# Kernel tuning notes

Hardware: AMD Instinct MI355X
Metric: run time of the kernel (lower is better)

## Reference

```python
import jax, jax.numpy as jnp
import numpy as np

B, S, D, H = 2, 2048, 1024, 16
HD = D // H  # head_dim = 64


def setup_inputs() -> dict:
    key = jax.random.key(0)
    ks = jax.random.split(key, 6)
    scale = D ** -0.5
    x = jax.random.normal(ks[0], (B, S, D), dtype=jnp.float32)
    wq = jax.random.normal(ks[1], (D, D), dtype=jnp.float32) * scale
    wk = jax.random.normal(ks[2], (D, D), dtype=jnp.float32) * scale
    wv = jax.random.normal(ks[3], (D, D), dtype=jnp.float32) * scale
    wo = jax.random.normal(ks[4], (D, D), dtype=jnp.float32) * scale
    # RoPE frequencies: theta_i = 10000^(-2i/HD), angles[t, i] = t * theta_i
    inv_freq = 1.0 / (10000.0 ** (np.arange(0, HD, 2, dtype=np.float32) / HD))
    t = np.arange(S, dtype=np.float32)
    angles = np.outer(t, inv_freq)  # [S, HD//2]
    freqs_cos = jnp.asarray(np.cos(angles), dtype=jnp.float32)
    freqs_sin = jnp.asarray(np.sin(angles), dtype=jnp.float32)
    # additive causal mask [1,1,S,S]
    neg = jnp.float32(-1e9)
    mask = jnp.triu(jnp.full((S, S), neg, dtype=jnp.float32), k=1)[None, None]
    return {"x": x, "wq": wq, "wk": wk, "wv": wv, "wo": wo,
            "freqs_cos": freqs_cos, "freqs_sin": freqs_sin,
            "mask": mask, "start_pos": 0}


def _apply_rope(q, freqs_cos, freqs_sin):
    # q: [B, S, H, HD] -> pairs (even, odd) rotated by angle per position
    b, s, h, hd = q.shape
    q2 = q.reshape(b, s, h, hd // 2, 2)
    qr, qi = q2[..., 0], q2[..., 1]
    c = freqs_cos[None, :, None, :]  # [1, S, 1, HD//2]
    sn = freqs_sin[None, :, None, :]
    out_r = qr * c - qi * sn
    out_i = qr * sn + qi * c
    return jnp.stack([out_r, out_i], axis=-1).reshape(b, s, h, hd)


def reference(x, wq, wk, wv, wo, freqs_cos, freqs_sin, mask, start_pos):
    b, s, _ = x.shape
    xq = (x @ wq).reshape(b, s, H, HD)
    xk = (x @ wk).reshape(b, s, H, HD)
    xv = (x @ wv).reshape(b, s, H, HD)
    xq = _apply_rope(xq, freqs_cos, freqs_sin)
    xk = _apply_rope(xk, freqs_cos, freqs_sin)
    # [B, H, S, HD]
    q = xq.transpose(0, 2, 1, 3)
    k = xk.transpose(0, 2, 1, 3)
    v = xv.transpose(0, 2, 1, 3)
    scores = jnp.einsum('bhqd,bhkd->bhqk', q, k) / jnp.sqrt(jnp.float32(HD))
    scores = scores + mask
    probs = jax.nn.softmax(scores.astype(jnp.float32), axis=-1).astype(q.dtype)
    out = jnp.einsum('bhqk,bhkd->bhqd', probs, v)
    out = out.transpose(0, 2, 1, 3).reshape(b, s, H * HD)
    return out @ wo
```

## Files before the change

### kernel.cpp

```cpp
#include <hip/hip_runtime.h>

typedef unsigned short u16;
typedef __bf16 bf16x8 __attribute__((ext_vector_type(8)));
typedef float f32x4 __attribute__((ext_vector_type(4)));

#define DD 1024
#define SS 2048
#define HH 16
#define HDIM 64

__device__ __forceinline__ u16 f2bf(float f) {
  union { float f; unsigned u; } x; x.f = f;
  unsigned r = x.u + 0x7FFFu + ((x.u >> 16) & 1u);
  return (u16)(r >> 16);
}

__device__ __forceinline__ void gload_lds16(const u16* g, u16* l) {
  __builtin_amdgcn_global_load_lds((const __attribute__((address_space(1))) void*)g,
                                   (__attribute__((address_space(3))) void*)l, 16, 0, 0);
}

__global__ __launch_bounds__(256) void cvt_x(const float* __restrict__ in, u16* __restrict__ out, int n) {
  int i = (blockIdx.x * 256 + threadIdx.x) * 4;
  if (i + 3 < n) {
    float4 v = *(const float4*)(in + i);
    out[i + 0] = f2bf(v.x);
    out[i + 1] = f2bf(v.y);
    out[i + 2] = f2bf(v.z);
    out[i + 3] = f2bf(v.w);
  }
}

__global__ __launch_bounds__(256) void transpose_w(const float* __restrict__ w0, const float* __restrict__ w1,
                                                   const float* __restrict__ w2, const float* __restrict__ w3,
                                                   u16* __restrict__ out) {
  __shared__ float t[32][33];
  const float* w = (blockIdx.z == 0) ? w0 : (blockIdx.z == 1) ? w1 : (blockIdx.z == 2) ? w2 : w3;
  u16* o = out + (size_t)blockIdx.z * DD * DD;
  int j0 = blockIdx.x * 32;
  int i0 = blockIdx.y * 32;
  int tx = threadIdx.x, ty = threadIdx.y;
#pragma unroll
  for (int r = ty; r < 32; r += 8)
    t[r][tx] = w[(size_t)(i0 + r) * DD + j0 + tx];
  __syncthreads();
#pragma unroll
  for (int r = ty; r < 32; r += 8)
    o[(size_t)(j0 + r) * DD + i0 + tx] = f2bf(t[tx][r]);
}

__device__ __forceinline__ void gemm_128(const u16* __restrict__ A, const u16* __restrict__ BT,
                                         int m0, int n0, int K, u16* As, u16* Bs, f32x4 acc[4][4]) {
  const int tid = threadIdx.x;
  const int lane = tid & 63;
  const int wid = tid >> 6;
  const int wm = wid >> 1, wn = wid & 1;
  const int lr = lane & 15;
  const int lg = lane >> 4;
#pragma unroll
  for (int i = 0; i < 4; ++i)
#pragma unroll
    for (int j = 0; j < 4; ++j)
      acc[i][j] = (f32x4){0.f, 0.f, 0.f, 0.f};

  for (int kt = 0; kt < K / 64; ++kt) {
    int k0 = kt * 64;
    __syncthreads();
#pragma unroll
    for (int i = 0; i < 4; ++i) {
      int c = i * 256 + tid;
      int row = c >> 3;
      int j = (c & 7) ^ (row & 7);
      gload_lds16(A + (size_t)(m0 + row) * K + k0 + j * 8, As + c * 8);
      gload_lds16(BT + (size_t)(n0 + row) * K + k0 + j * 8, Bs + c * 8);
    }
    __syncthreads();
#pragma unroll
    for (int ks = 0; ks < 2; ++ks) {
      bf16x8 af[4], bfr[4];
#pragma unroll
      for (int mi = 0; mi < 4; ++mi) {
        int row = wm * 64 + mi * 16 + lr;
        int ch = (ks * 4 + lg) ^ (row & 7);
        af[mi] = *(const bf16x8*)(As + row * 64 + ch * 8);
      }
#pragma unroll
      for (int ni = 0; ni < 4; ++ni) {
        int row = wn * 64 + ni * 16 + lr;
        int ch = (ks * 4 + lg) ^ (row & 7);
        bfr[ni] = *(const bf16x8*)(Bs + row * 64 + ch * 8);
      }
      __builtin_amdgcn_s_setprio(1);
#pragma unroll
      for (int mi = 0; mi < 4; ++mi)
#pragma unroll
        for (int ni = 0; ni < 4; ++ni)
          acc[mi][ni] = __builtin_amdgcn_mfma_f32_16x16x32_bf16(af[mi], bfr[ni], acc[mi][ni], 0, 0, 0);
      __builtin_amdgcn_s_setprio(0);
    }
  }
}

__global__ __launch_bounds__(256, 2) void gemm_qkv(const u16* __restrict__ xb, const u16* __restrict__ wT,
                                                   const float* __restrict__ fc, const float* __restrict__ fs,
                                                   u16* __restrict__ Qr, u16* __restrict__ Kr, u16* __restrict__ Vt) {
  __shared__ u16 As[128 * 64], Bs[128 * 64];
  const int z = blockIdx.z;
  const u16* BT = wT + (size_t)z * DD * DD;
  f32x4 acc[4][4];
  int m0 = blockIdx.x * 128, n0 = blockIdx.y * 128;
  gemm_128(xb, BT, m0, n0, DD, As, Bs, acc);

  const int lane = threadIdx.x & 63, wid = threadIdx.x >> 6;
  const int wm = wid >> 1, wn = wid & 1, lr = lane & 15, lg = lane >> 4;
#pragma unroll
  for (int mi = 0; mi < 4; ++mi)
#pragma unroll
    for (int ni = 0; ni < 4; ++ni)
#pragma unroll
      for (int j = 0; j < 4; ++j) {
        int m = m0 + wm * 64 + mi * 16 + lg * 4 + j;
        int n = n0 + wn * 64 + ni * 16 + lr;
        float v = acc[mi][ni][j];
        int b = m >> 11, s = m & 2047;
        int h = n >> 6, hd = n & 63;
        if (z == 2) {
          Vt[((size_t)(b * HH + h) * HDIM + hd) * SS + s] = f2bf(v);
        } else {
          float pv = __shfl_xor(v, 1);
          int fi = s * 32 + (hd >> 1);
          float c = fc[fi], sn = fs[fi];
          float o = ((hd & 1) == 0) ? (v * c - pv * sn) : (pv * sn + v * c);
          u16* dst = (z == 0) ? Qr : Kr;
          dst[((size_t)(b * HH + h) * SS + s) * HDIM + hd] = f2bf(o);
        }
      }
}

__global__ __launch_bounds__(256, 4) void attn(const u16* __restrict__ Qr, const u16* __restrict__ Kr,
                                               const u16* __restrict__ Vt, u16* __restrict__ Ob) {
  __shared__ u16 Kb[2][64 * 64];
  __shared__ u16 Vb[2][64 * 64];
  __shared__ u16 Ps[4][16 * 64];
  const int id = blockIdx.x;
  const int xcd = id & 7;
  const int r = id >> 3;
  const int qt = 31 - (r >> 2);
  const int bh = xcd * 4 + (r & 3);

  const u16* Qh = Qr + (size_t)bh * SS * HDIM;
  const u16* Kh = Kr + (size_t)bh * SS * HDIM;
  const u16* Vh = Vt + (size_t)bh * HDIM * SS;

  const int tid = threadIdx.x;
  const int lane = tid & 63, wid = tid >> 6;
  const int lr = lane & 15, lg = lane >> 4;
  const int q0 = qt * 64 + wid * 16;
  u16* Pw = &Ps[wid][0];

  const int c0 = tid, c1 = 256 + tid;
  const int srow0 = c0 >> 3, sj0 = (c0 & 7) ^ (srow0 & 7);
  const int srow1 = c1 >> 3, sj1 = (c1 & 7) ^ (srow1 & 7);

  bf16x8 aq[2];
#pragma unroll
  for (int ks = 0; ks < 2; ++ks)
    aq[ks] = *(const bf16x8*)(Qh + (q0 + lr) * HDIM + ks * 32 + lg * 8);

  bf16x8 ones;
  {
    union { u16 u[8]; bf16x8 v; } ou;
#pragma unroll
    for (int i = 0; i < 8; ++i) ou.u[i] = 0x3F80;
    ones = ou.v;
  }

  f32x4 o[4];
#pragma unroll
  for (int d = 0; d < 4; ++d) o[d] = (f32x4){0.f, 0.f, 0.f, 0.f};
  f32x4 ls = (f32x4){0.f, 0.f, 0.f, 0.f};

  gload_lds16(Kh + (size_t)srow0 * HDIM + sj0 * 8, &Kb[0][c0 * 8]);
  gload_lds16(Kh + (size_t)srow1 * HDIM + sj1 * 8, &Kb[0][c1 * 8]);
  gload_lds16(Vh + (size_t)srow0 * SS + sj0 * 8, &Vb[0][c0 * 8]);
  gload_lds16(Vh + (size_t)srow1 * SS + sj1 * 8, &Vb[0][c1 * 8]);

  for (int t = 0; t <= qt; ++t) {
    const int cur = t & 1;
    __syncthreads();

    if (t < qt) {
      const int g0 = (t + 1) * 64;
      gload_lds16(Kh + (size_t)(g0 + srow0) * HDIM + sj0 * 8, &Kb[cur ^ 1][c0 * 8]);
      gload_lds16(Kh + (size_t)(g0 + srow1) * HDIM + sj1 * 8, &Kb[cur ^ 1][c1 * 8]);
      gload_lds16(Vh + (size_t)srow0 * SS + g0 + sj0 * 8, &Vb[cur ^ 1][c0 * 8]);
      gload_lds16(Vh + (size_t)srow1 * SS + g0 + sj1 * 8, &Vb[cur ^ 1][c1 * 8]);
    }

    f32x4 sc[4];
#pragma unroll
    for (int kb = 0; kb < 4; ++kb) sc[kb] = (f32x4){0.f, 0.f, 0.f, 0.f};
    __builtin_amdgcn_s_setprio(1);
#pragma unroll
    for (int ks = 0; ks < 2; ++ks)
#pragma unroll
      for (int kb = 0; kb < 4; ++kb) {
        int row = kb * 16 + lr;
        int ch = (ks * 4 + lg) ^ (row & 7);
        bf16x8 bk = *(const bf16x8*)(&Kb[cur][row * 64 + ch * 8]);
        sc[kb] = __builtin_amdgcn_mfma_f32_16x16x32_bf16(aq[ks], bk, sc[kb], 0, 0, 0);
      }
    __builtin_amdgcn_s_setprio(0);

    if (t == qt) {
#pragma unroll
      for (int kb = 0; kb < 4; ++kb)
#pragma unroll
        for (int j = 0; j < 4; ++j) {
          int q = q0 + lg * 4 + j;
          int kk = t * 64 + kb * 16 + lr;
          float e = __expf(sc[kb][j] * 0.125f);
          sc[kb][j] = (kk > q) ? 0.f : e;
        }
    } else {
#pragma unroll
      for (int kb = 0; kb < 4; ++kb)
#pragma unroll
        for (int j = 0; j < 4; ++j)
          sc[kb][j] = __expf(sc[kb][j] * 0.125f);
    }

#pragma unroll
    for (int kb = 0; kb < 4; ++kb)
#pragma unroll
      for (int j = 0; j < 4; ++j) {
        int rr = lg * 4 + j;
        int ccol = kb * 16 + lr;
        int ch = (ccol >> 3) ^ (rr & 7);
        Pw[rr * 64 + ch * 8 + (ccol & 7)] = f2bf(sc[kb][j]);
      }
#pragma unroll
    for (int ks = 0; ks < 2; ++ks) {
      int chp = (ks * 4 + lg) ^ (lr & 7);
      bf16x8 ap = *(const bf16x8*)(Pw + lr * 64 + chp * 8);
      __builtin_amdgcn_s_setprio(1);
      ls = __builtin_amdgcn_mfma_f32_16x16x32_bf16(ap, ones, ls, 0, 0, 0);
#pragma unroll
      for (int d = 0; d < 4; ++d) {
        int row = d * 16 + lr;
        int ch = (ks * 4 + lg) ^ (row & 7);
        bf16x8 bv = *(const bf16x8*)(&Vb[cur][row * 64 + ch * 8]);
        o[d] = __builtin_amdgcn_mfma_f32_16x16x32_bf16(ap, bv, o[d], 0, 0, 0);
      }
      __builtin_amdgcn_s_setprio(0);
    }
  }

  const int b = bh >> 4, h = bh & 15;
#pragma unroll
  for (int d = 0; d < 4; ++d)
#pragma unroll
    for (int j = 0; j < 4; ++j) {
      int s = q0 + lg * 4 + j;
      int col = h * HDIM + d * 16 + lr;
      Ob[((size_t)b * SS + s) * DD + col] = f2bf(o[d][j] / ls[j]);
    }
}

__global__ __launch_bounds__(256, 2) void gemm_wo(const u16* __restrict__ Ab, const u16* __restrict__ woT,
                                                  float* __restrict__ out) {
  __shared__ u16 As[128 * 64], Bs[128 * 64];
  f32x4 acc[4][4];
  int m0 = blockIdx.x * 128, n0 = blockIdx.y * 128;
  gemm_128(Ab, woT, m0, n0, DD, As, Bs, acc);
  const int lane = threadIdx.x & 63, wid = threadIdx.x >> 6;
  const int wm = wid >> 1, wn = wid & 1, lr = lane & 15, lg = lane >> 4;
#pragma unroll
  for (int mi = 0; mi < 4; ++mi)
#pragma unroll
    for (int ni = 0; ni < 4; ++ni)
#pragma unroll
      for (int j = 0; j < 4; ++j) {
        int m = m0 + wm * 64 + mi * 16 + lg * 4 + j;
        int n = n0 + wn * 64 + ni * 16 + lr;
        out[(size_t)m * DD + n] = acc[mi][ni][j];
      }
}

extern "C" void kernel_launch(void* const* d_in, const int* in_sizes, int n_in,
                              void* d_out, int out_size, void* d_ws, size_t ws_size,
                              hipStream_t stream) {
  const float* x  = (const float*)d_in[0];
  const float* wq = (const float*)d_in[1];
  const float* wk = (const float*)d_in[2];
  const float* wv = (const float*)d_in[3];
  const float* wo = (const float*)d_in[4];
  const float* fc = (const float*)d_in[5];
  const float* fs = (const float*)d_in[6];
  float* out = (float*)d_out;

  char* ws = (char*)d_ws;
  u16* xb = (u16*)(ws);
  u16* wT = (u16*)(ws + (8ull << 20));
  u16* Qr = (u16*)(ws + (16ull << 20));
  u16* Kr = (u16*)(ws + (24ull << 20));
  u16* Vt = (u16*)(ws + (32ull << 20));
  u16* Ob = (u16*)(ws + (40ull << 20));

  cvt_x<<<4096, 256, 0, stream>>>(x, xb, 4096 * 1024);
  transpose_w<<<dim3(32, 32, 4), dim3(32, 8), 0, stream>>>(wq, wk, wv, wo, wT);
  gemm_qkv<<<dim3(32, 8, 3), 256, 0, stream>>>(xb, wT, fc, fs, Qr, Kr, Vt);
  attn<<<1024, 256, 0, stream>>>(Qr, Kr, Vt, Ob);
  gemm_wo<<<dim3(32, 8), 256, 0, stream>>>(Ob, wT + 3ull * DD * DD, out);
}
```

Measured before the change: 122.3 us.

## Split attention KV loop across two wave groups and pair causal query tiles

The attention kernel now runs 512-thread blocks. Two groups of four waves each process alternating 64-key tiles from a shared 128-key staged block, then merge their partial outputs and row sums through LDS. Each block handles a query tile and its mirror (pair, 31-pair) so causal work is balanced across blocks. The kernel also switches the P-matrix bf16 conversion to the hardware v_cvt_pk_bf16_f32 instruction. In exchange it uses more LDS and adds an extra reduction and sync step, and the odd/even tile split wastes a masked tile when the count is odd.

```diff
diff --git a/kernel.cpp b/kernel.cpp
--- a/kernel.cpp
+++ b/kernel.cpp
@@ -13,6 +13,12 @@
   union { float f; unsigned u; } x; x.f = f;
   unsigned r = x.u + 0x7FFFu + ((x.u >> 16) & 1u);
   return (u16)(r >> 16);
+}
+
+__device__ __forceinline__ u16 f2bf_s(float f) {
+  unsigned r;
+  asm("v_cvt_pk_bf16_f32 %0, %1, %2" : "=v"(r) : "v"(f), "v"(0.f));
+  return (u16)r;
 }
 
 __device__ __forceinline__ void gload_lds16(const u16* g, u16* l) {
@@ -137,30 +143,26 @@
       }
 }
 
-__global__ __launch_bounds__(256, 4) void attn(const u16* __restrict__ Qr, const u16* __restrict__ Kr,
-                                               const u16* __restrict__ Vt, u16* __restrict__ Ob) {
-  __shared__ u16 Kb[2][64 * 64];
-  __shared__ u16 Vb[2][64 * 64];
-  __shared__ u16 Ps[4][16 * 64];
-  const int id = blockIdx.x;
-  const int xcd = id & 7;
-  const int r = id >> 3;
-  const int qt = 31 - (r >> 2);
-  const int bh = xcd * 4 + (r & 3);
-
-  const u16* Qh = Qr + (size_t)bh * SS * HDIM;
-  const u16* Kh = Kr + (size_t)bh * SS * HDIM;
-  const u16* Vh = Vt + (size_t)bh * HDIM * SS;
-
+__device__ __forceinline__ void stage_tile(const u16* __restrict__ Kh, const u16* __restrict__ Vh,
+                                           int i2, u16* Kbuf, u16* Vbuf, int tid) {
+#pragma unroll
+  for (int k = 0; k < 2; ++k) {
+    const int c = tid + k * 512;
+    const int tt = c >> 9, cl = c & 511;
+    const int row = cl >> 3, j = (cl & 7) ^ (row & 7);
+    gload_lds16(Kh + (size_t)(i2 * 128 + tt * 64 + row) * HDIM + j * 8, Kbuf + c * 8);
+    gload_lds16(Vh + (size_t)row * SS + i2 * 128 + tt * 64 + j * 8, Vbuf + c * 8);
+  }
+}
+
+__device__ __forceinline__ void attn_pass(int qt, int bh, const u16* __restrict__ Qh,
+                                          const u16* __restrict__ Kh, const u16* __restrict__ Vh,
+                                          u16* __restrict__ Ob, u16* KbR, u16* VbR, u16* Pw,
+                                          int gid, int wq) {
   const int tid = threadIdx.x;
-  const int lane = tid & 63, wid = tid >> 6;
+  const int lane = tid & 63;
   const int lr = lane & 15, lg = lane >> 4;
-  const int q0 = qt * 64 + wid * 16;
-  u16* Pw = &Ps[wid][0];
-
-  const int c0 = tid, c1 = 256 + tid;
-  const int srow0 = c0 >> 3, sj0 = (c0 & 7) ^ (srow0 & 7);
-  const int srow1 = c1 >> 3, sj1 = (c1 & 7) ^ (srow1 & 7);
+  const int q0 = qt * 64 + wq * 16;
 
   bf16x8 aq[2];
 #pragma unroll
@@ -180,22 +182,19 @@
   for (int d = 0; d < 4; ++d) o[d] = (f32x4){0.f, 0.f, 0.f, 0.f};
   f32x4 ls = (f32x4){0.f, 0.f, 0.f, 0.f};
 
-  gload_lds16(Kh + (size_t)srow0 * HDIM + sj0 * 8, &Kb[0][c0 * 8]);
-  gload_lds16(Kh + (size_t)srow1 * HDIM + sj1 * 8, &Kb[0][c1 * 8]);
-  gload_lds16(Vh + (size_t)srow0 * SS + sj0 * 8, &Vb[0][c0 * 8]);
-  gload_lds16(Vh + (size_t)srow1 * SS + sj1 * 8, &Vb[0][c1 * 8]);
-
-  for (int t = 0; t <= qt; ++t) {
-    const int cur = t & 1;
+  const int n2 = (qt + 2) >> 1;
+
+  __syncthreads();
+  stage_tile(Kh, Vh, 0, KbR, VbR, tid);
+
+  for (int i = 0; i < n2; ++i) {
+    const int cur = i & 1;
     __syncthreads();
-
-    if (t < qt) {
-      const int g0 = (t + 1) * 64;
-      gload_lds16(Kh + (size_t)(g0 + srow0) * HDIM + sj0 * 8, &Kb[cur ^ 1][c0 * 8]);
-      gload_lds16(Kh + (size_t)(g0 + srow1) * HDIM + sj1 * 8, &Kb[cur ^ 1][c1 * 8]);
-      gload_lds16(Vh + (size_t)srow0 * SS + g0 + sj0 * 8, &Vb[cur ^ 1][c0 * 8]);
-      gload_lds16(Vh + (size_t)srow1 * SS + g0 + sj1 * 8, &Vb[cur ^ 1][c1 * 8]);
-    }
+    if (i + 1 < n2) stage_tile(Kh, Vh, i + 1, KbR + (cur ^ 1) * 8192, VbR + (cur ^ 1) * 8192, tid);
+
+    const int t = 2 * i + gid;
+    const u16* Kt = KbR + cur * 8192 + gid * 4096;
+    const u16* Vtl = VbR + cur * 8192 + gid * 4096;
 
     f32x4 sc[4];
 #pragma unroll
@@ -207,12 +206,12 @@
       for (int kb = 0; kb < 4; ++kb) {
         int row = kb * 16 + lr;
         int ch = (ks * 4 + lg) ^ (row & 7);
-        bf16x8 bk = *(const bf16x8*)(&Kb[cur][row * 64 + ch * 8]);
+        bf16x8 bk = *(const bf16x8*)(Kt + row * 64 + ch * 8);
         sc[kb] = __builtin_amdgcn_mfma_f32_16x16x32_bf16(aq[ks], bk, sc[kb], 0, 0, 0);
       }
     __builtin_amdgcn_s_setprio(0);
 
-    if (t == qt) {
+    if (t >= qt) {
 #pragma unroll
       for (int kb = 0; kb < 4; ++kb)
 #pragma unroll
@@ -237,7 +236,7 @@
         int rr = lg * 4 + j;
         int ccol = kb * 16 + lr;
         int ch = (ccol >> 3) ^ (rr & 7);
-        Pw[rr * 64 + ch * 8 + (ccol & 7)] = f2bf(sc[kb][j]);
+        Pw[rr * 64 + ch * 8 + (ccol & 7)] = f2bf_s(sc[kb][j]);
       }
 #pragma unroll
     for (int ks = 0; ks < 2; ++ks) {
@@ -249,22 +248,62 @@
       for (int d = 0; d < 4; ++d) {
         int row = d * 16 + lr;
         int ch = (ks * 4 + lg) ^ (row & 7);
-        bf16x8 bv = *(const bf16x8*)(&Vb[cur][row * 64 + ch * 8]);
+        bf16x8 bv = *(const bf16x8*)(Vtl + row * 64 + ch * 8);
         o[d] = __builtin_amdgcn_mfma_f32_16x16x32_bf16(ap, bv, o[d], 0, 0, 0);
       }
       __builtin_amdgcn_s_setprio(0);
     }
   }
 
-  const int b = bh >> 4, h = bh & 15;
-#pragma unroll
-  for (int d = 0; d < 4; ++d)
-#pragma unroll
-    for (int j = 0; j < 4; ++j) {
-      int s = q0 + lg * 4 + j;
-      int col = h * HDIM + d * 16 + lr;
-      Ob[((size_t)b * SS + s) * DD + col] = f2bf(o[d][j] / ls[j]);
-    }
+  __syncthreads();
+  float* mo = (float*)KbR;
+  float* ml = (float*)VbR;
+  if (gid == 1) {
+#pragma unroll
+    for (int d = 0; d < 4; ++d)
+#pragma unroll
+      for (int j = 0; j < 4; ++j)
+        mo[(wq * 16 + lg * 4 + j) * 64 + d * 16 + lr] = o[d][j];
+    if (lr == 0) {
+#pragma unroll
+      for (int j = 0; j < 4; ++j) ml[wq * 16 + lg * 4 + j] = ls[j];
+    }
+  }
+  __syncthreads();
+  if (gid == 0) {
+    const int b = bh >> 4, h = bh & 15;
+#pragma unroll
+    for (int j = 0; j < 4; ++j) ls[j] += ml[wq * 16 + lg * 4 + j];
+#pragma unroll
+    for (int d = 0; d < 4; ++d)
+#pragma unroll
+      for (int j = 0; j < 4; ++j) {
+        float val = o[d][j] + mo[(wq * 16 + lg * 4 + j) * 64 + d * 16 + lr];
+        int s = q0 + lg * 4 + j;
+        int col = h * HDIM + d * 16 + lr;
+        Ob[((size_t)b * SS + s) * DD + col] = f2bf(val / ls[j]);
+      }
+  }
+}
+
+__global__ __launch_bounds__(512, 4) void attn(const u16* __restrict__ Qr, const u16* __restrict__ Kr,
+                                               const u16* __restrict__ Vt, u16* __restrict__ Ob) {
+  __shared__ u16 Kb[2][2][64 * 64];
+  __shared__ u16 Vb[2][2][64 * 64];
+  __shared__ u16 Ps[8][16 * 64];
+  const int id = blockIdx.x;
+  const int xcd = id & 7;
+  const int r = id >> 3;
+  const int pair = r & 15;
+  const int bh = xcd * 4 + (r >> 4);
+  const u16* Qh = Qr + (size_t)bh * SS * HDIM;
+  const u16* Kh = Kr + (size_t)bh * SS * HDIM;
+  const u16* Vh = Vt + (size_t)bh * HDIM * SS;
+  const int wid = threadIdx.x >> 6;
+  const int gid = wid >> 2, wq = wid & 3;
+  u16* Pw = &Ps[wid][0];
+  attn_pass(pair, bh, Qh, Kh, Vh, Ob, &Kb[0][0][0], &Vb[0][0][0], Pw, gid, wq);
+  attn_pass(31 - pair, bh, Qh, Kh, Vh, Ob, &Kb[0][0][0], &Vb[0][0][0], Pw, gid, wq);
 }
 
 __global__ __launch_bounds__(256, 2) void gemm_wo(const u16* __restrict__ Ab, const u16* __restrict__ woT,
@@ -310,6 +349,6 @@
   cvt_x<<<4096, 256, 0, stream>>>(x, xb, 4096 * 1024);
   transpose_w<<<dim3(32, 32, 4), dim3(32, 8), 0, stream>>>(wq, wk, wv, wo, wT);
   gemm_qkv<<<dim3(32, 8, 3), 256, 0, stream>>>(xb, wT, fc, fs, Qr, Kr, Vt);
-  attn<<<1024, 256, 0, stream>>>(Qr, Kr, Vt, Ob);
+  attn<<<512, 512, 0, stream>>>(Qr, Kr, Vt, Ob);
   gemm_wo<<<dim3(32, 8), 256, 0, stream>>>(Ob, wT + 3ull * DD * DD, out);
 }
```

Result: no change. 120.0 us (-1.9%).
